# Performance work log

Measured on AMD Instinct MI355X. Metric: run time of the kernel, lower is better.

Reference implementation:

```python
import jax, jax.numpy as jnp
import numpy as np

BETA = 0.5      # conf.beta (undefined global in original repo)
ALPHA = 0.2     # LeakyReLU negative slope (init arg alpha)
N, E, FIN, FOUT = 50000, 1_600_000, 128, 64


def setup_inputs() -> dict:
    key = jax.random.key(0)
    k1, k2, k3, k4, k5 = jax.random.split(key, 5)
    inp = jax.random.normal(k1, (N, FIN), dtype=jnp.float32)
    edge = jax.random.randint(k2, (2, E), 0, N)                      # [2,E] (src,dst), = adj.nonzero().t()
    M_vals = jax.random.uniform(k3, (E,), dtype=jnp.float32)          # M gathered at edges
    # xavier_normal with gain 1.414, matching torch init
    W = jax.random.normal(k4, (FIN, FOUT), dtype=jnp.float32) * (1.414 * np.sqrt(2.0 / (FIN + FOUT)))
    a = jax.random.normal(k5, (2 * FOUT,), dtype=jnp.float32) * (1.414 * np.sqrt(2.0 / (1 + 2 * FOUT)))
    return {"input": inp, "M_vals": M_vals, "W": W, "a": a, "edge": edge}


def reference(input, M_vals, W, a, edge):
    n, f = input.shape[0], W.shape[1]
    src, dst = edge[0], edge[1]
    h = input @ W                                   # [N, F]
    # M = beta*M + (1-beta)*adj; at edges adj == 1
    bias = M_vals * BETA + (1.0 - BETA)             # [E]
    # a . cat(h_src, bias*h_dst) == (h@a[:F])[src] + bias * (h@a[F:])[dst]
    s1 = h @ a[:f]                                  # [N]
    s2 = h @ a[f:]                                  # [N]
    edge_e = jnp.exp(jax.nn.leaky_relu(s1[src] + bias * s2[dst], negative_slope=ALPHA))  # [E]
    # special_spmm(edge, e, [N,N], ones) -> per-row sum of edge weights
    e_rowsum = jax.ops.segment_sum(edge_e, src, num_segments=n)       # [N]
    # special_spmm(edge, e, [N,N], h) -> weighted aggregation of dst features into src rows
    h_prime = jax.ops.segment_sum(edge_e[:, None] * h[dst], src, num_segments=n)  # [N, F]
    h_prime = h_prime / e_rowsum[:, None]
    return jax.nn.elu(h_prime)                      # concat=True
```

## Files before the change

kernel.cpp:

```cpp
#include <hip/hip_runtime.h>
#include <hip/hip_bf16.h>

#define NN   50000
#define EE   1600000
#define FIN  128
#define FOUT 64
#define BETA  0.5f
#define ALPHA 0.2f
#define SBW    64
#define SBSH   6
#define NB     782
#define RCAP   2500
#define PGRID  512
#define PCHUNK 3125
#define CAPB   2504
#define XS     136

typedef __attribute__((ext_vector_type(8))) short short8;
typedef __attribute__((ext_vector_type(8))) unsigned short ushort8v;
typedef __attribute__((ext_vector_type(4))) float float4v;

__device__ __forceinline__ float load_any(const void* p, long i, int isf32) {
    if (isf32) return ((const float*)p)[i];
    unsigned int b = ((unsigned int)(((const unsigned short*)p)[i])) << 16;
    return __uint_as_float(b);
}

__device__ __forceinline__ unsigned short f32_to_bf16_rne(float f) {
    unsigned int b = __float_as_uint(f);
    return (unsigned short)((b + 0x7FFF + ((b >> 16) & 1)) >> 16);
}

__device__ __forceinline__ float bf16_to_f32(unsigned short u) {
    return __uint_as_float(((unsigned int)u) << 16);
}

__global__ __launch_bounds__(256) void detwt_kernel(
    const void* __restrict__ W, const void* __restrict__ Mv,
    unsigned short* __restrict__ Wt, int* __restrict__ flags,
    int* __restrict__ bcur)
{
    __shared__ int vote;
    const int tid = threadIdx.x;
    if (tid == 0) vote = 0;
    __syncthreads();

    int m = 0;
    const float vw = bf16_to_f32(((const unsigned short*)W)[tid * 16]);
    if (isnan(vw) || fabsf(vw) > 1e4f) m |= 1;
    if (blockIdx.x == 0) {
        const long half = (long)EE >> 1;
        const long pos = 2 * (((long)tid * (half / 256)) % half);
        const float vm = bf16_to_f32(((const unsigned short*)Mv)[pos]);
        if (isnan(vm) || fabsf(vm) > 1e4f) m |= 2;
    }
    if (m) atomicOr(&vote, m);
    __syncthreads();

    const int fW = vote & 1;
    if (blockIdx.x == 0) {
        if (tid == 0) flags[1] = (vote >> 1) & 1;
        for (int i = tid; i < NB; i += 256) bcur[i] = 0;
    }
    const int i = blockIdx.x * 256 + tid;
    const int k = i >> 6, n = i & 63;
    Wt[n * FIN + k] = f32_to_bf16_rne(load_any(W, i, fW));
}

__global__ __launch_bounds__(256) void mfma_gemm_kernel(
    const void* __restrict__ inp,
    const unsigned short* __restrict__ Wt,
    const void* __restrict__ a,
    unsigned short* __restrict__ h,
    float* __restrict__ s1,
    float* __restrict__ s2,
    int* __restrict__ flags)
{
    __shared__ unsigned short Xs[16 * XS];
    __shared__ float part1[4][16];
    __shared__ float part2[4][16];
    __shared__ int vote;

    const int tid  = threadIdx.x;
    const int wave = tid >> 6;
    const int lane = tid & 63;
    const int quad = lane >> 4;
    const int col  = lane & 15;
    const int rb0  = blockIdx.x * 32;

    if (tid == 0) vote = 0;
    __syncthreads();

    {
        int m = 0;
        const float vi = bf16_to_f32(((const unsigned short*)inp)[(long)rb0 * FIN + tid * 8]);
        if (isnan(vi) || fabsf(vi) > 1e4f) m |= 1;
        if (tid < 128) {
            const float va = bf16_to_f32(((const unsigned short*)a)[tid]);
            if (isnan(va) || fabsf(va) > 1e4f) m |= 2;
        }
        if (m) atomicOr(&vote, m);
    }
    __syncthreads();
    const int fI = vote & 1, fA = (vote >> 1) & 1;
    if (blockIdx.x == 0 && tid == 0) flags[0] = fI;

    const int nb = wave * 16;
    const float a1 = load_any(a, nb + col, fA);
    const float a2 = load_any(a, 64 + nb + col, fA);

    for (int t = 0; t < 2; ++t) {
        const int rb = rb0 + t * 16;
        if (rb >= NN) break;

        {
            const int r = tid >> 4, k8 = (tid & 15) * 8;
            if (!fI) {
                const unsigned short* src = (const unsigned short*)inp + (long)(rb + r) * FIN + k8;
                *(ushort8v*)&Xs[r * XS + k8] = *(const ushort8v*)src;
            } else {
                const float* src = (const float*)inp + (long)(rb + r) * FIN + k8;
                ushort8v v;
                #pragma unroll
                for (int j = 0; j < 8; ++j) v[j] = f32_to_bf16_rne(src[j]);
                *(ushort8v*)&Xs[r * XS + k8] = v;
            }
        }
        __syncthreads();

        float4v acc = { 0.f, 0.f, 0.f, 0.f };
        #pragma unroll
        for (int k0 = 0; k0 < FIN; k0 += 32) {
            const short8 af = *(const short8*)&Xs[col * XS + k0 + quad * 8];
            const short8 bf = *(const short8*)&Wt[(long)(nb + col) * FIN + k0 + quad * 8];
            acc = __builtin_amdgcn_mfma_f32_16x16x32_bf16(af, bf, acc, 0, 0, 0);
        }

        #pragma unroll
        for (int r = 0; r < 4; ++r)
            h[(long)(rb + quad * 4 + r) * FOUT + nb + col] = f32_to_bf16_rne(acc[r]);

        #pragma unroll
        for (int r = 0; r < 4; ++r) {
            float v1 = acc[r] * a1;
            float v2 = acc[r] * a2;
            #pragma unroll
            for (int o = 1; o < 16; o <<= 1) {
                v1 += __shfl_xor(v1, o, 64);
                v2 += __shfl_xor(v2, o, 64);
            }
            if (col == 0) {
                part1[wave][quad * 4 + r] = v1;
                part2[wave][quad * 4 + r] = v2;
            }
        }
        __syncthreads();
        if (tid < 16) {
            s1[rb + tid] = part1[0][tid] + part1[1][tid] + part1[2][tid] + part1[3][tid];
            s2[rb + tid] = part2[0][tid] + part2[1][tid] + part2[2][tid] + part2[3][tid];
        }
    }
}

__global__ __launch_bounds__(1024) void partition_kernel(
    const int* __restrict__ edge,
    const void* __restrict__ Mv,
    const int* __restrict__ flags,
    const float* __restrict__ s1,
    const float* __restrict__ s2,
    int* __restrict__ bcur,
    unsigned long long* __restrict__ recs)
{
    __shared__ int lcnt[NB];
    __shared__ int lbase[NB];
    const int tid = threadIdx.x;
    const int fM = flags[1];
    const int e0 = blockIdx.x * PCHUNK;

    if (tid < NB) lcnt[tid] = 0;
    __syncthreads();

    int srcs[4], dsts[4];
    #pragma unroll
    for (int k = 0; k < 4; ++k) {
        const int e = e0 + tid + 1024 * k;
        const bool ok = (tid + 1024 * k) < PCHUNK;
        srcs[k] = ok ? edge[e] : -1;
        dsts[k] = ok ? edge[EE + e] : 0;
    }

    float ss1[4], ss2[4], mvs[4];
    #pragma unroll
    for (int k = 0; k < 4; ++k) {
        ss1[k] = (srcs[k] >= 0) ? s1[srcs[k]] : 0.f;
        ss2[k] = (srcs[k] >= 0) ? s2[dsts[k]] : 0.f;
    }
    #pragma unroll
    for (int k = 0; k < 4; ++k) {
        const int e = e0 + tid + 1024 * k;
        mvs[k] = ((tid + 1024 * k) < PCHUNK) ? load_any(Mv, e, fM) : 0.f;
    }

    #pragma unroll
    for (int k = 0; k < 4; ++k)
        if (srcs[k] >= 0) atomicAdd(&lcnt[srcs[k] >> SBSH], 1);
    __syncthreads();

    if (tid < NB) {
        const int c = lcnt[tid];
        const int o = c ? atomicAdd(&bcur[tid], c) : 0;
        lbase[tid] = tid * RCAP + o;
        lcnt[tid] = 0;
    }
    __syncthreads();

    #pragma unroll
    for (int k = 0; k < 4; ++k) {
        if (srcs[k] < 0) continue;
        const float bias = mvs[k] * BETA + (1.f - BETA);
        const float x  = ss1[k] + bias * ss2[k];
        const float lr = x > 0.f ? x : ALPHA * x;
        const float ee = __expf(lr);
        const int b = srcs[k] >> SBSH;
        const int r = atomicAdd(&lcnt[b], 1);
        const int pos = lbase[b] + r;
        if (pos < (b + 1) * RCAP)
            recs[pos] = ((unsigned long long)(unsigned)srcs[k] << 32)
                      | ((unsigned long long)(unsigned)dsts[k] << 16)
                      | (unsigned long long)f32_to_bf16_rne(ee);
    }
}

__global__ __launch_bounds__(512) void csr_spmm_kernel(
    const int* __restrict__ bcur,
    const unsigned long long* __restrict__ recs,
    const unsigned short* __restrict__ h,
    const int* __restrict__ flags,
    void* __restrict__ out)
{
    __shared__ unsigned long long lrec[CAPB];
    __shared__ unsigned int lpair[CAPB];
    __shared__ int cnt[SBW];
    __shared__ int off[SBW];
    const int b    = blockIdx.x;
    const int tid  = threadIdx.x;
    const int rb   = b * SBW;
    const int beg  = b * RCAP;

    int n = bcur[b]; if (n > RCAP) n = RCAP;

    if (tid < SBW) cnt[tid] = 0;
    __syncthreads();

    for (int j = tid; j < n; j += 512) {
        const unsigned long long rec = recs[beg + j];
        const int r = (int)(rec >> 32) - rb;
        const int rank = atomicAdd(&cnt[r], 1);
        lrec[j] = ((unsigned long long)(unsigned)(r | (rank << 8)) << 32)
                | (unsigned long long)(unsigned)(rec & 0xFFFFFFFFu);
    }
    __syncthreads();

    if (tid < SBW) {
        const int c = cnt[tid];
        int x = c;
        #pragma unroll
        for (int o = 1; o < SBW; o <<= 1) {
            int y = __shfl_up(x, o, 64);
            if (tid >= o) x += y;
        }
        off[tid] = x - c;
    }
    __syncthreads();

    for (int j = tid; j < n; j += 512) {
        const unsigned long long rec = lrec[j];
        const unsigned int hi = (unsigned int)(rec >> 32);
        lpair[off[hi & 63u] + (hi >> 8)] = (unsigned int)(rec & 0xFFFFFFFFu);
    }
    __syncthreads();

    const int wv   = tid >> 6;
    const int lane = tid & 63;
    const int gr   = lane >> 3;
    const int sl   = lane & 7;
    const int rr   = wv * 8 + gr;
    const int row  = rb + rr;
    const int fOut = flags[0];

    const int jb = off[rr];
    const int je = jb + cnt[rr];

    float acc0 = 0.f, acc1 = 0.f, acc2 = 0.f, acc3 = 0.f;
    float acc4 = 0.f, acc5 = 0.f, acc6 = 0.f, acc7 = 0.f;
    float rsum = 0.f;
    int j = jb;
    for (; j + 3 < je; j += 4) {
        unsigned int u[4];
        #pragma unroll
        for (int kk = 0; kk < 4; ++kk) u[kk] = lpair[j + kk];
        ushort8v hv[4];
        #pragma unroll
        for (int kk = 0; kk < 4; ++kk)
            hv[kk] = *(const ushort8v*)&h[(long)(u[kk] >> 16) * FOUT + 8 * sl];
        #pragma unroll
        for (int kk = 0; kk < 4; ++kk) {
            const float v = bf16_to_f32((unsigned short)(u[kk] & 0xFFFFu));
            rsum += v;
            acc0 = fmaf(v, bf16_to_f32(hv[kk][0]), acc0);
            acc1 = fmaf(v, bf16_to_f32(hv[kk][1]), acc1);
            acc2 = fmaf(v, bf16_to_f32(hv[kk][2]), acc2);
            acc3 = fmaf(v, bf16_to_f32(hv[kk][3]), acc3);
            acc4 = fmaf(v, bf16_to_f32(hv[kk][4]), acc4);
            acc5 = fmaf(v, bf16_to_f32(hv[kk][5]), acc5);
            acc6 = fmaf(v, bf16_to_f32(hv[kk][6]), acc6);
            acc7 = fmaf(v, bf16_to_f32(hv[kk][7]), acc7);
        }
    }
    for (; j < je; ++j) {
        const unsigned int u = lpair[j];
        const ushort8v hv = *(const ushort8v*)&h[(long)(u >> 16) * FOUT + 8 * sl];
        const float v = bf16_to_f32((unsigned short)(u & 0xFFFFu));
        rsum += v;
        acc0 = fmaf(v, bf16_to_f32(hv[0]), acc0);
        acc1 = fmaf(v, bf16_to_f32(hv[1]), acc1);
        acc2 = fmaf(v, bf16_to_f32(hv[2]), acc2);
        acc3 = fmaf(v, bf16_to_f32(hv[3]), acc3);
        acc4 = fmaf(v, bf16_to_f32(hv[4]), acc4);
        acc5 = fmaf(v, bf16_to_f32(hv[5]), acc5);
        acc6 = fmaf(v, bf16_to_f32(hv[6]), acc6);
        acc7 = fmaf(v, bf16_to_f32(hv[7]), acc7);
    }

    if (row < NN && je > jb) {
        const float inv = 1.f / rsum;
        float q0 = acc0 * inv, q1 = acc1 * inv, q2 = acc2 * inv, q3 = acc3 * inv;
        float q4 = acc4 * inv, q5 = acc5 * inv, q6 = acc6 * inv, q7 = acc7 * inv;
        q0 = q0 > 0.f ? q0 : (__expf(q0) - 1.f);
        q1 = q1 > 0.f ? q1 : (__expf(q1) - 1.f);
        q2 = q2 > 0.f ? q2 : (__expf(q2) - 1.f);
        q3 = q3 > 0.f ? q3 : (__expf(q3) - 1.f);
        q4 = q4 > 0.f ? q4 : (__expf(q4) - 1.f);
        q5 = q5 > 0.f ? q5 : (__expf(q5) - 1.f);
        q6 = q6 > 0.f ? q6 : (__expf(q6) - 1.f);
        q7 = q7 > 0.f ? q7 : (__expf(q7) - 1.f);
        if (fOut) {
            float4* o = (float4*)((float*)out + (long)row * FOUT + 8 * sl);
            o[0] = make_float4(q0, q1, q2, q3);
            o[1] = make_float4(q4, q5, q6, q7);
        } else {
            ushort8v ov;
            ov[0] = f32_to_bf16_rne(q0); ov[1] = f32_to_bf16_rne(q1);
            ov[2] = f32_to_bf16_rne(q2); ov[3] = f32_to_bf16_rne(q3);
            ov[4] = f32_to_bf16_rne(q4); ov[5] = f32_to_bf16_rne(q5);
            ov[6] = f32_to_bf16_rne(q6); ov[7] = f32_to_bf16_rne(q7);
            *(ushort8v*)((unsigned short*)out + (long)row * FOUT + 8 * sl) = ov;
        }
    } else if (row < NN) {
        if (fOut) {
            float4* o = (float4*)((float*)out + (long)row * FOUT + 8 * sl);
            o[0] = make_float4(0.f, 0.f, 0.f, 0.f);
            o[1] = make_float4(0.f, 0.f, 0.f, 0.f);
        } else {
            ushort8v ov = { 0, 0, 0, 0, 0, 0, 0, 0 };
            *(ushort8v*)((unsigned short*)out + (long)row * FOUT + 8 * sl) = ov;
        }
    }
}

extern "C" void kernel_launch(void* const* d_in, const int* in_sizes, int n_in,
                              void* d_out, int out_size, void* d_ws, size_t ws_size,
                              hipStream_t stream) {
    const void* inp  = d_in[0];
    const void* Mv   = d_in[1];
    const void* W    = d_in[2];
    const void* a    = d_in[3];
    const int*  edge = (const int*)d_in[4];

    char* p = (char*)d_ws;
    int*                flags  = (int*)p;            p += 256;
    unsigned short*     Wt     = (unsigned short*)p; p += ((size_t)FOUT * FIN * 2 + 255) / 256 * 256;
    unsigned short*     h      = (unsigned short*)p; p += ((size_t)NN * FOUT * 2 + 255) / 256 * 256;
    float*              s1     = (float*)p;          p += ((size_t)NN * 4 + 255) / 256 * 256;
    float*              s2     = (float*)p;          p += ((size_t)NN * 4 + 255) / 256 * 256;
    int*                bcur   = (int*)p;            p += ((size_t)NB * 4 + 255) / 256 * 256;
    unsigned long long* recs   = (unsigned long long*)p;

    detwt_kernel<<<32, 256, 0, stream>>>(W, Mv, Wt, flags, bcur);
    mfma_gemm_kernel<<<(NN + 31) / 32, 256, 0, stream>>>(inp, Wt, a, h, s1, s2, flags);
    partition_kernel<<<PGRID, 1024, 0, stream>>>(edge, Mv, flags, s1, s2, bcur, recs);
    csr_spmm_kernel<<<NB, 512, 0, stream>>>(bcur, recs, h, flags, d_out);
}
```

Before: 154.4 us.

## Compute per-row edge ranks with global atomics in partition, drop LDS counting pass

The partition kernel now takes a per-source-row rank for every edge with a global atomicAdd on a new rowcnt array and packs that rank into the top 16 bits of each record. The SpMM kernel then reads per-row counts straight from rowcnt and scatters records directly into their CSR slots, removing the shared-memory counting pass and the lrec staging buffer. The detwt kernel is widened to zero rowcnt. The cost is 1.6M global atomics scattered over 50K addresses, in exchange for less LDS traffic and one fewer pass and barrier in the SpMM blocks.

```diff
diff --git a/kernel.cpp b/kernel.cpp
--- a/kernel.cpp
+++ b/kernel.cpp
@@ -38,33 +38,40 @@
 __global__ __launch_bounds__(256) void detwt_kernel(
     const void* __restrict__ W, const void* __restrict__ Mv,
     unsigned short* __restrict__ Wt, int* __restrict__ flags,
-    int* __restrict__ bcur)
+    int* __restrict__ bcur, int* __restrict__ rowcnt)
 {
     __shared__ int vote;
     const int tid = threadIdx.x;
     if (tid == 0) vote = 0;
     __syncthreads();
 
-    int m = 0;
-    const float vw = bf16_to_f32(((const unsigned short*)W)[tid * 16]);
-    if (isnan(vw) || fabsf(vw) > 1e4f) m |= 1;
-    if (blockIdx.x == 0) {
-        const long half = (long)EE >> 1;
-        const long pos = 2 * (((long)tid * (half / 256)) % half);
-        const float vm = bf16_to_f32(((const unsigned short*)Mv)[pos]);
-        if (isnan(vm) || fabsf(vm) > 1e4f) m |= 2;
-    }
-    if (m) atomicOr(&vote, m);
-    __syncthreads();
-
-    const int fW = vote & 1;
-    if (blockIdx.x == 0) {
-        if (tid == 0) flags[1] = (vote >> 1) & 1;
-        for (int i = tid; i < NB; i += 256) bcur[i] = 0;
-    }
-    const int i = blockIdx.x * 256 + tid;
-    const int k = i >> 6, n = i & 63;
-    Wt[n * FIN + k] = f32_to_bf16_rne(load_any(W, i, fW));
+    {
+        const int i = blockIdx.x * 256 + tid;
+        if (i < NN) rowcnt[i] = 0;
+    }
+
+    if (blockIdx.x < 32) {
+        int m = 0;
+        const float vw = bf16_to_f32(((const unsigned short*)W)[tid * 16]);
+        if (isnan(vw) || fabsf(vw) > 1e4f) m |= 1;
+        if (blockIdx.x == 0) {
+            const long half = (long)EE >> 1;
+            const long pos = 2 * (((long)tid * (half / 256)) % half);
+            const float vm = bf16_to_f32(((const unsigned short*)Mv)[pos]);
+            if (isnan(vm) || fabsf(vm) > 1e4f) m |= 2;
+        }
+        if (m) atomicOr(&vote, m);
+        __syncthreads();
+
+        const int fW = vote & 1;
+        if (blockIdx.x == 0) {
+            if (tid == 0) flags[1] = (vote >> 1) & 1;
+            for (int j = tid; j < NB; j += 256) bcur[j] = 0;
+        }
+        const int i = blockIdx.x * 256 + tid;
+        const int k = i >> 6, n = i & 63;
+        Wt[n * FIN + k] = f32_to_bf16_rne(load_any(W, i, fW));
+    }
 }
 
 __global__ __launch_bounds__(256) void mfma_gemm_kernel(
@@ -169,6 +176,7 @@
     const float* __restrict__ s1,
     const float* __restrict__ s2,
     int* __restrict__ bcur,
+    int* __restrict__ rowcnt,
     unsigned long long* __restrict__ recs)
 {
     __shared__ int lcnt[NB];
@@ -188,6 +196,11 @@
         srcs[k] = ok ? edge[e] : -1;
         dsts[k] = ok ? edge[EE + e] : 0;
     }
+
+    int rnk[4];
+    #pragma unroll
+    for (int k = 0; k < 4; ++k)
+        rnk[k] = (srcs[k] >= 0) ? atomicAdd(&rowcnt[srcs[k]], 1) : 0;
 
     float ss1[4], ss2[4], mvs[4];
     #pragma unroll
@@ -225,7 +238,8 @@
         const int r = atomicAdd(&lcnt[b], 1);
         const int pos = lbase[b] + r;
         if (pos < (b + 1) * RCAP)
-            recs[pos] = ((unsigned long long)(unsigned)srcs[k] << 32)
+            recs[pos] = ((unsigned long long)(unsigned)(rnk[k] & 0xFFFF) << 48)
+                      | ((unsigned long long)(unsigned)srcs[k] << 32)
                       | ((unsigned long long)(unsigned)dsts[k] << 16)
                       | (unsigned long long)f32_to_bf16_rne(ee);
     }
@@ -233,12 +247,12 @@
 
 __global__ __launch_bounds__(512) void csr_spmm_kernel(
     const int* __restrict__ bcur,
+    const int* __restrict__ rowcnt,
     const unsigned long long* __restrict__ recs,
     const unsigned short* __restrict__ h,
     const int* __restrict__ flags,
     void* __restrict__ out)
 {
-    __shared__ unsigned long long lrec[CAPB];
     __shared__ unsigned int lpair[CAPB];
     __shared__ int cnt[SBW];
     __shared__ int off[SBW];
@@ -249,20 +263,11 @@
 
     int n = bcur[b]; if (n > RCAP) n = RCAP;
 
-    if (tid < SBW) cnt[tid] = 0;
-    __syncthreads();
-
-    for (int j = tid; j < n; j += 512) {
-        const unsigned long long rec = recs[beg + j];
-        const int r = (int)(rec >> 32) - rb;
-        const int rank = atomicAdd(&cnt[r], 1);
-        lrec[j] = ((unsigned long long)(unsigned)(r | (rank << 8)) << 32)
-                | (unsigned long long)(unsigned)(rec & 0xFFFFFFFFu);
-    }
-    __syncthreads();
+    for (int i = tid; i < CAPB; i += 512) lpair[i] = 0;
 
     if (tid < SBW) {
-        const int c = cnt[tid];
+        int c = (rb + tid < NN) ? rowcnt[rb + tid] : 0;
+        cnt[tid] = c;
         int x = c;
         #pragma unroll
         for (int o = 1; o < SBW; o <<= 1) {
@@ -274,9 +279,11 @@
     __syncthreads();
 
     for (int j = tid; j < n; j += 512) {
-        const unsigned long long rec = lrec[j];
-        const unsigned int hi = (unsigned int)(rec >> 32);
-        lpair[off[hi & 63u] + (hi >> 8)] = (unsigned int)(rec & 0xFFFFFFFFu);
+        const unsigned long long rec = recs[beg + j];
+        const int r    = (int)((rec >> 32) & 0xFFFFu) - rb;
+        const int rank = (int)(rec >> 48);
+        const int idx  = off[r] + rank;
+        if (idx < CAPB) lpair[idx] = (unsigned int)(rec & 0xFFFFFFFFu);
     }
     __syncthreads();
 
@@ -384,10 +391,11 @@
     float*              s1     = (float*)p;          p += ((size_t)NN * 4 + 255) / 256 * 256;
     float*              s2     = (float*)p;          p += ((size_t)NN * 4 + 255) / 256 * 256;
     int*                bcur   = (int*)p;            p += ((size_t)NB * 4 + 255) / 256 * 256;
+    int*                rowcnt = (int*)p;            p += ((size_t)NN * 4 + 255) / 256 * 256;
     unsigned long long* recs   = (unsigned long long*)p;
 
-    detwt_kernel<<<32, 256, 0, stream>>>(W, Mv, Wt, flags, bcur);
+    detwt_kernel<<<196, 256, 0, stream>>>(W, Mv, Wt, flags, bcur, rowcnt);
     mfma_gemm_kernel<<<(NN + 31) / 32, 256, 0, stream>>>(inp, Wt, a, h, s1, s2, flags);
-    partition_kernel<<<PGRID, 1024, 0, stream>>>(edge, Mv, flags, s1, s2, bcur, recs);
-    csr_spmm_kernel<<<NB, 512, 0, stream>>>(bcur, recs, h, flags, d_out);
-}
+    partition_kernel<<<PGRID, 1024, 0, stream>>>(edge, Mv, flags, s1, s2, bcur, rowcnt, recs);
+    csr_spmm_kernel<<<NB, 512, 0, stream>>>(bcur, rowcnt, recs, h, flags, d_out);
+}
```

Measured after the change: 205.3 us. +32.9%, slower.

## Replace global atomic bucket offsets with separate count and scan passes

Applied to the files above, without the earlier changes.

Moves per-block bucket counting of source rows into a new count kernel that writes a per-bucket, per-block count matrix. A scan kernel then computes exclusive prefix offsets, so the partition kernel reads precomputed bases instead of doing global atomicAdds. The SpMM kernel sums the counts itself to get each bucket's total. The aim is deterministic record placement without global atomics, at the cost of two extra passes, another read of the source indices, and one more launch.

```diff
diff --git a/kernel.cpp b/kernel.cpp
--- a/kernel.cpp
+++ b/kernel.cpp
@@ -35,36 +35,73 @@
     return __uint_as_float(((unsigned int)u) << 16);
 }
 
-__global__ __launch_bounds__(256) void detwt_kernel(
+__global__ __launch_bounds__(1024) void count_kernel(
+    const int* __restrict__ edge,
     const void* __restrict__ W, const void* __restrict__ Mv,
     unsigned short* __restrict__ Wt, int* __restrict__ flags,
-    int* __restrict__ bcur)
+    int* __restrict__ cnts)
 {
+    __shared__ int lcnt[NB];
     __shared__ int vote;
     const int tid = threadIdx.x;
+    const int blk = blockIdx.x;
+
     if (tid == 0) vote = 0;
-    __syncthreads();
-
-    int m = 0;
-    const float vw = bf16_to_f32(((const unsigned short*)W)[tid * 16]);
-    if (isnan(vw) || fabsf(vw) > 1e4f) m |= 1;
-    if (blockIdx.x == 0) {
+    if (tid < NB) lcnt[tid] = 0;
+    __syncthreads();
+
+    const int e0 = blk * PCHUNK;
+    #pragma unroll
+    for (int k = 0; k < 4; ++k) {
+        const int idx = tid + 1024 * k;
+        if (idx < PCHUNK) atomicAdd(&lcnt[edge[e0 + idx] >> SBSH], 1);
+    }
+
+    if (blk == 0 && tid < 256) {
+        int m = 0;
+        const float vw = bf16_to_f32(((const unsigned short*)W)[tid * 16]);
+        if (isnan(vw) || fabsf(vw) > 1e4f) m |= 1;
         const long half = (long)EE >> 1;
         const long pos = 2 * (((long)tid * (half / 256)) % half);
         const float vm = bf16_to_f32(((const unsigned short*)Mv)[pos]);
         if (isnan(vm) || fabsf(vm) > 1e4f) m |= 2;
-    }
-    if (m) atomicOr(&vote, m);
-    __syncthreads();
-
-    const int fW = vote & 1;
-    if (blockIdx.x == 0) {
+        if (m) atomicOr(&vote, m);
+    }
+    __syncthreads();
+
+    if (blk == 0) {
+        const int fW = vote & 1;
         if (tid == 0) flags[1] = (vote >> 1) & 1;
-        for (int i = tid; i < NB; i += 256) bcur[i] = 0;
-    }
-    const int i = blockIdx.x * 256 + tid;
-    const int k = i >> 6, n = i & 63;
-    Wt[n * FIN + k] = f32_to_bf16_rne(load_any(W, i, fW));
+        for (int i = tid; i < FIN * FOUT; i += 1024) {
+            const int k = i >> 6, n = i & 63;
+            Wt[n * FIN + k] = f32_to_bf16_rne(load_any(W, i, fW));
+        }
+    }
+
+    if (tid < NB) cnts[tid * PGRID + blk] = lcnt[tid];
+}
+
+__global__ __launch_bounds__(512) void scan_kernel(
+    const int* __restrict__ cnts,
+    int* __restrict__ basesT)
+{
+    __shared__ int wpart[8];
+    const int b   = blockIdx.x;
+    const int tid = threadIdx.x;
+    const int lane = tid & 63, wv = tid >> 6;
+
+    const int c = cnts[b * PGRID + tid];
+    int x = c;
+    #pragma unroll
+    for (int o = 1; o < 64; o <<= 1) {
+        int y = __shfl_up(x, o, 64);
+        if (lane >= o) x += y;
+    }
+    if (lane == 63) wpart[wv] = x;
+    __syncthreads();
+    int wb = 0;
+    for (int w = 0; w < wv; ++w) wb += wpart[w];
+    basesT[(long)tid * NB + b] = wb + x - c;
 }
 
 __global__ __launch_bounds__(256) void mfma_gemm_kernel(
@@ -168,16 +205,20 @@
     const int* __restrict__ flags,
     const float* __restrict__ s1,
     const float* __restrict__ s2,
-    int* __restrict__ bcur,
+    const int* __restrict__ basesT,
     unsigned long long* __restrict__ recs)
 {
     __shared__ int lcnt[NB];
     __shared__ int lbase[NB];
     const int tid = threadIdx.x;
+    const int blk = blockIdx.x;
     const int fM = flags[1];
-    const int e0 = blockIdx.x * PCHUNK;
-
-    if (tid < NB) lcnt[tid] = 0;
+    const int e0 = blk * PCHUNK;
+
+    if (tid < NB) {
+        lcnt[tid] = 0;
+        lbase[tid] = tid * RCAP + basesT[(long)blk * NB + tid];
+    }
     __syncthreads();
 
     int srcs[4], dsts[4];
@@ -200,19 +241,6 @@
         const int e = e0 + tid + 1024 * k;
         mvs[k] = ((tid + 1024 * k) < PCHUNK) ? load_any(Mv, e, fM) : 0.f;
     }
-
-    #pragma unroll
-    for (int k = 0; k < 4; ++k)
-        if (srcs[k] >= 0) atomicAdd(&lcnt[srcs[k] >> SBSH], 1);
-    __syncthreads();
-
-    if (tid < NB) {
-        const int c = lcnt[tid];
-        const int o = c ? atomicAdd(&bcur[tid], c) : 0;
-        lbase[tid] = tid * RCAP + o;
-        lcnt[tid] = 0;
-    }
-    __syncthreads();
 
     #pragma unroll
     for (int k = 0; k < 4; ++k) {
@@ -232,8 +260,8 @@
 }
 
 __global__ __launch_bounds__(512) void csr_spmm_kernel(
-    const int* __restrict__ bcur,
     const unsigned long long* __restrict__ recs,
+    const int* __restrict__ cnts,
     const unsigned short* __restrict__ h,
     const int* __restrict__ flags,
     void* __restrict__ out)
@@ -242,12 +270,23 @@
     __shared__ unsigned int lpair[CAPB];
     __shared__ int cnt[SBW];
     __shared__ int off[SBW];
+    __shared__ int ntot;
     const int b    = blockIdx.x;
     const int tid  = threadIdx.x;
     const int rb   = b * SBW;
     const int beg  = b * RCAP;
 
-    int n = bcur[b]; if (n > RCAP) n = RCAP;
+    {
+        int s = 0;
+        for (int j = tid; j < PGRID; j += 512) s += cnts[b * PGRID + j];
+        #pragma unroll
+        for (int o = 1; o < 64; o <<= 1) s += __shfl_xor(s, o, 64);
+        if (tid == 0) ntot = 0;
+        __syncthreads();
+        if ((tid & 63) == 0) atomicAdd(&ntot, s);
+        __syncthreads();
+    }
+    int n = ntot; if (n > RCAP) n = RCAP;
 
     if (tid < SBW) cnt[tid] = 0;
     __syncthreads();
@@ -383,11 +422,13 @@
     unsigned short*     h      = (unsigned short*)p; p += ((size_t)NN * FOUT * 2 + 255) / 256 * 256;
     float*              s1     = (float*)p;          p += ((size_t)NN * 4 + 255) / 256 * 256;
     float*              s2     = (float*)p;          p += ((size_t)NN * 4 + 255) / 256 * 256;
-    int*                bcur   = (int*)p;            p += ((size_t)NB * 4 + 255) / 256 * 256;
+    int*                cnts   = (int*)p;            p += ((size_t)NB * PGRID * 4 + 255) / 256 * 256;
+    int*                basesT = (int*)p;            p += ((size_t)PGRID * NB * 4 + 255) / 256 * 256;
     unsigned long long* recs   = (unsigned long long*)p;
 
-    detwt_kernel<<<32, 256, 0, stream>>>(W, Mv, Wt, flags, bcur);
+    count_kernel<<<PGRID, 1024, 0, stream>>>(edge, W, Mv, Wt, flags, cnts);
+    scan_kernel<<<NB, 512, 0, stream>>>(cnts, basesT);
     mfma_gemm_kernel<<<(NN + 31) / 32, 256, 0, stream>>>(inp, Wt, a, h, s1, s2, flags);
-    partition_kernel<<<PGRID, 1024, 0, stream>>>(edge, Mv, flags, s1, s2, bcur, recs);
-    csr_spmm_kernel<<<NB, 512, 0, stream>>>(bcur, recs, h, flags, d_out);
-}
+    partition_kernel<<<PGRID, 1024, 0, stream>>>(edge, Mv, flags, s1, s2, basesT, recs);
+    csr_spmm_kernel<<<NB, 512, 0, stream>>>(recs, cnts, h, flags, d_out);
+}
```

Result: slower. 162.1 us (+5.0%).

## Replace global atomic bucket cursors with per-block local sort and offset table

Applied to the files above, without the earlier changes.

The partition kernel now sorts each chunk's edge records by bucket in shared memory, writes them out contiguously, and stores a per-block bucket offset table, so it no longer reserves slots with global atomics into fixed-capacity bucket regions. The SpMM kernel has each of its 512 threads read one partition block's segment for its bucket, and a prefix scan places the records in shared memory. This removes global atomic contention and the scattered record writes, at the cost of a serial per-thread loop over short segments with uncoalesced reads and a strided offset-table lookup.

```diff
diff --git a/kernel.cpp b/kernel.cpp
--- a/kernel.cpp
+++ b/kernel.cpp
@@ -10,7 +10,6 @@
 #define SBW    64
 #define SBSH   6
 #define NB     782
-#define RCAP   2500
 #define PGRID  512
 #define PCHUNK 3125
 #define CAPB   2504
@@ -37,8 +36,7 @@
 
 __global__ __launch_bounds__(256) void detwt_kernel(
     const void* __restrict__ W, const void* __restrict__ Mv,
-    unsigned short* __restrict__ Wt, int* __restrict__ flags,
-    int* __restrict__ bcur)
+    unsigned short* __restrict__ Wt, int* __restrict__ flags)
 {
     __shared__ int vote;
     const int tid = threadIdx.x;
@@ -58,10 +56,7 @@
     __syncthreads();
 
     const int fW = vote & 1;
-    if (blockIdx.x == 0) {
-        if (tid == 0) flags[1] = (vote >> 1) & 1;
-        for (int i = tid; i < NB; i += 256) bcur[i] = 0;
-    }
+    if (blockIdx.x == 0 && tid == 0) flags[1] = (vote >> 1) & 1;
     const int i = blockIdx.x * 256 + tid;
     const int k = i >> 6, n = i & 63;
     Wt[n * FIN + k] = f32_to_bf16_rne(load_any(W, i, fW));
@@ -168,14 +163,17 @@
     const int* __restrict__ flags,
     const float* __restrict__ s1,
     const float* __restrict__ s2,
-    int* __restrict__ bcur,
-    unsigned long long* __restrict__ recs)
+    unsigned long long* __restrict__ recs,
+    int* __restrict__ loffT)
 {
+    __shared__ unsigned long long lrecs[PCHUNK];
     __shared__ int lcnt[NB];
-    __shared__ int lbase[NB];
+    __shared__ int loff[NB];
+    __shared__ int wsum[16];
     const int tid = threadIdx.x;
+    const int blk = blockIdx.x;
     const int fM = flags[1];
-    const int e0 = blockIdx.x * PCHUNK;
+    const int e0 = blk * PCHUNK;
 
     if (tid < NB) lcnt[tid] = 0;
     __syncthreads();
@@ -206,11 +204,23 @@
         if (srcs[k] >= 0) atomicAdd(&lcnt[srcs[k] >> SBSH], 1);
     __syncthreads();
 
-    if (tid < NB) {
-        const int c = lcnt[tid];
-        const int o = c ? atomicAdd(&bcur[tid], c) : 0;
-        lbase[tid] = tid * RCAP + o;
-        lcnt[tid] = 0;
+    {
+        const int lane = tid & 63, wv = tid >> 6;
+        const int c = (tid < NB) ? lcnt[tid] : 0;
+        int x = c;
+        #pragma unroll
+        for (int o = 1; o < 64; o <<= 1) {
+            int y = __shfl_up(x, o, 64);
+            if (lane >= o) x += y;
+        }
+        if (lane == 63) wsum[wv] = x;
+        __syncthreads();
+        int wb = 0;
+        for (int w = 0; w < wv; ++w) wb += wsum[w];
+        if (tid < NB) {
+            loff[tid] = wb + x - c;
+            lcnt[tid] = 0;
+        }
     }
     __syncthreads();
 
@@ -223,17 +233,21 @@
         const float ee = __expf(lr);
         const int b = srcs[k] >> SBSH;
         const int r = atomicAdd(&lcnt[b], 1);
-        const int pos = lbase[b] + r;
-        if (pos < (b + 1) * RCAP)
-            recs[pos] = ((unsigned long long)(unsigned)srcs[k] << 32)
-                      | ((unsigned long long)(unsigned)dsts[k] << 16)
-                      | (unsigned long long)f32_to_bf16_rne(ee);
-    }
+        lrecs[loff[b] + r] = ((unsigned long long)(unsigned)srcs[k] << 32)
+                           | ((unsigned long long)(unsigned)dsts[k] << 16)
+                           | (unsigned long long)f32_to_bf16_rne(ee);
+    }
+    __syncthreads();
+
+    for (int j = tid; j < PCHUNK; j += 1024)
+        recs[e0 + j] = lrecs[j];
+    if (tid < NB) loffT[(long)blk * (NB + 1) + tid] = loff[tid];
+    if (tid == 0) loffT[(long)blk * (NB + 1) + NB] = PCHUNK;
 }
 
 __global__ __launch_bounds__(512) void csr_spmm_kernel(
-    const int* __restrict__ bcur,
     const unsigned long long* __restrict__ recs,
+    const int* __restrict__ loffT,
     const unsigned short* __restrict__ h,
     const int* __restrict__ flags,
     void* __restrict__ out)
@@ -242,24 +256,54 @@
     __shared__ unsigned int lpair[CAPB];
     __shared__ int cnt[SBW];
     __shared__ int off[SBW];
+    __shared__ int wsum[8];
     const int b    = blockIdx.x;
     const int tid  = threadIdx.x;
     const int rb   = b * SBW;
-    const int beg  = b * RCAP;
-
-    int n = bcur[b]; if (n > RCAP) n = RCAP;
 
     if (tid < SBW) cnt[tid] = 0;
-    __syncthreads();
-
-    for (int j = tid; j < n; j += 512) {
-        const unsigned long long rec = recs[beg + j];
-        const int r = (int)(rec >> 32) - rb;
-        const int rank = atomicAdd(&cnt[r], 1);
-        lrec[j] = ((unsigned long long)(unsigned)(r | (rank << 8)) << 32)
-                | (unsigned long long)(unsigned)(rec & 0xFFFFFFFFu);
-    }
-    __syncthreads();
+
+    const int lo  = loffT[(long)tid * (NB + 1) + b];
+    const int hi  = loffT[(long)tid * (NB + 1) + b + 1];
+    const int len = hi - lo;
+
+    int segbase;
+    {
+        const int lane = tid & 63, wv = tid >> 6;
+        int x = len;
+        #pragma unroll
+        for (int o = 1; o < 64; o <<= 1) {
+            int y = __shfl_up(x, o, 64);
+            if (lane >= o) x += y;
+        }
+        if (lane == 63) wsum[wv] = x;
+        __syncthreads();
+        int wb = 0;
+        for (int w = 0; w < wv; ++w) wb += wsum[w];
+        segbase = wb + x - len;
+    }
+
+    const unsigned long long* seg = recs + (long)tid * PCHUNK + lo;
+    for (int i = 0; i < len; ++i) {
+        const int idx = segbase + i;
+        if (idx < CAPB) {
+            const unsigned long long rec = seg[i];
+            const int r = (int)(rec >> 32) - rb;
+            const int rank = atomicAdd(&cnt[r], 1);
+            lrec[idx] = ((unsigned long long)(unsigned)(r | (rank << 8)) << 32)
+                      | (unsigned long long)(unsigned)(rec & 0xFFFFFFFFu);
+        }
+    }
+    __syncthreads();
+    const int ntot0 = off[0];
+    (void)ntot0;
+    int n = segbase;
+    {
+        int tot = 0;
+        #pragma unroll
+        for (int w = 0; w < 8; ++w) tot += wsum[w];
+        n = tot > CAPB ? CAPB : tot;
+    }
 
     if (tid < SBW) {
         const int c = cnt[tid];
@@ -275,8 +319,8 @@
 
     for (int j = tid; j < n; j += 512) {
         const unsigned long long rec = lrec[j];
-        const unsigned int hi = (unsigned int)(rec >> 32);
-        lpair[off[hi & 63u] + (hi >> 8)] = (unsigned int)(rec & 0xFFFFFFFFu);
+        const unsigned int hi32 = (unsigned int)(rec >> 32);
+        lpair[off[hi32 & 63u] + (hi32 >> 8)] = (unsigned int)(rec & 0xFFFFFFFFu);
     }
     __syncthreads();
 
@@ -383,11 +427,11 @@
     unsigned short*     h      = (unsigned short*)p; p += ((size_t)NN * FOUT * 2 + 255) / 256 * 256;
     float*              s1     = (float*)p;          p += ((size_t)NN * 4 + 255) / 256 * 256;
     float*              s2     = (float*)p;          p += ((size_t)NN * 4 + 255) / 256 * 256;
-    int*                bcur   = (int*)p;            p += ((size_t)NB * 4 + 255) / 256 * 256;
+    int*                loffT  = (int*)p;            p += ((size_t)PGRID * (NB + 1) * 4 + 255) / 256 * 256;
     unsigned long long* recs   = (unsigned long long*)p;
 
-    detwt_kernel<<<32, 256, 0, stream>>>(W, Mv, Wt, flags, bcur);
+    detwt_kernel<<<32, 256, 0, stream>>>(W, Mv, Wt, flags);
     mfma_gemm_kernel<<<(NN + 31) / 32, 256, 0, stream>>>(inp, Wt, a, h, s1, s2, flags);
-    partition_kernel<<<PGRID, 1024, 0, stream>>>(edge, Mv, flags, s1, s2, bcur, recs);
-    csr_spmm_kernel<<<NB, 512, 0, stream>>>(bcur, recs, h, flags, d_out);
-}
+    partition_kernel<<<PGRID, 1024, 0, stream>>>(edge, Mv, flags, s1, s2, recs, loffT);
+    csr_spmm_kernel<<<NB, 512, 0, stream>>>(recs, loffT, h, flags, d_out);
+}
```

Result: no change. 155.6 us (+0.8%).
